# Kernel optimization log

Hardware: AMD Instinct MI355X
Metric: run time of the kernel (lower is better)

## Reference

```python
import jax, jax.numpy as jnp
import numpy as np

B, T, C, NH, HS, NL, VOCAB = 4, 1024, 768, 12, 64, 6, 128
PRIMES = [2, 3, 5, 7, 11, 13, 17, 19, 23, 29]
NEG_INF = jnp.finfo(jnp.float32).min


def _build_lut(t):
    # lut[n, i] = v_{p_i}(n), p-adic valuation of position n
    lut = np.zeros((t + 1, len(PRIMES)), np.float32)
    for pi, p in enumerate(PRIMES):
        nn = np.arange(t + 1, dtype=np.int64)
        nn[0] = 1  # v_p(0) treated as 0
        while (nn % p == 0).any():
            d = nn % p == 0
            lut[d, pi] += 1.0
            nn[d] //= p
    return lut


def _build_buffers(t):
    lut = _build_lut(t)
    vl = lut[1 : t + 1]  # positions 1..T, [T, 10]
    res = np.minimum(vl[:, None, :], vl[None, :, :]).sum(-1)  # [T, T]
    causal = np.tril(np.ones((t, t), dtype=bool))
    allowed = ((res > 0) | np.eye(t, dtype=bool)) & causal
    rbias = (np.log1p(res) * allowed).astype(np.float32)
    return vl.astype(np.float32), rbias, allowed


def setup_inputs() -> dict:
    key = jax.random.key(0)
    ks = jax.random.split(key, 16)
    s = 0.02
    vl, rbias, allowed = _build_buffers(T)
    return {
        "idx": jax.random.randint(ks[0], (B, T), 0, VOCAB, dtype=jnp.int32),
        "tok_emb": jax.random.normal(ks[1], (VOCAB, C)) * s,
        "pe_w": jax.random.normal(ks[2], (10, C)) * s,
        "pe_b": jnp.zeros((C,)),
        "vlut": jnp.asarray(vl),
        "rbias": jnp.asarray(rbias),
        "allowed": jnp.asarray(allowed),
        "ln1_g": jnp.ones((NL, C)),
        "ln1_b": jnp.zeros((NL, C)),
        "qw": jax.random.normal(ks[3], (NL, NH, C, HS)) * s,
        "kw": jax.random.normal(ks[4], (NL, NH, C, HS)) * s,
        "vw": jax.random.normal(ks[5], (NL, NH, C, HS)) * s,
        "proj_w": jax.random.normal(ks[6], (NL, C, C)) * s,
        "proj_b": jnp.zeros((NL, C)),
        "ln2_g": jnp.ones((NL, C)),
        "ln2_b": jnp.zeros((NL, C)),
        "ff1_w": jax.random.normal(ks[7], (NL, C, 4 * C)) * s,
        "ff1_b": jnp.zeros((NL, 4 * C)),
        "ff2_w": jax.random.normal(ks[8], (NL, 4 * C, C)) * s,
        "ff2_b": jnp.zeros((NL, C)),
        "lnf_g": jnp.ones((C,)),
        "lnf_b": jnp.zeros((C,)),
        "head_w": jax.random.normal(ks[9], (C, VOCAB)) * s,
        "head_b": jnp.zeros((VOCAB,)),
    }


def _ln(x, g, b, eps=1e-5):
    m = x.mean(-1, keepdims=True)
    v = ((x - m) ** 2).mean(-1, keepdims=True)
    return (x - m) * jax.lax.rsqrt(v + eps) * g + b


def reference(idx, tok_emb, pe_w, pe_b, vlut, rbias, allowed,
              ln1_g, ln1_b, qw, kw, vw, proj_w, proj_b,
              ln2_g, ln2_b, ff1_w, ff1_b, ff2_w, ff2_b,
              lnf_g, lnf_b, head_w, head_b):
    # token embedding + spectral positional encoding
    x = tok_emb[idx] + (vlut @ pe_w + pe_b)  # [B, T, C]
    scale = C ** (-0.5)  # NOTE: source scales by full embed dim, not head_size
    for l in range(NL):
        h = _ln(x, ln1_g[l], ln1_b[l])
        q = jnp.einsum("btc,hcd->bhtd", h, qw[l])
        k = jnp.einsum("btc,hcd->bhtd", h, kw[l])
        v = jnp.einsum("btc,hcd->bhtd", h, vw[l])
        w = jnp.einsum("bhtd,bhsd->bhts", q, k) * scale + rbias  # [B,H,T,T]
        w = jnp.where(allowed, w, NEG_INF)
        a = jax.nn.softmax(w, axis=-1)
        o = jnp.einsum("bhts,bhsd->bhtd", a, v)
        o = o.transpose(0, 2, 1, 3).reshape(x.shape[0], x.shape[1], C)
        x = x + o @ proj_w[l] + proj_b[l]
        h2 = _ln(x, ln2_g[l], ln2_b[l])
        x = x + jax.nn.gelu(h2 @ ff1_w[l] + ff1_b[l], approximate=False) @ ff2_w[l] + ff2_b[l]
    return _ln(x, lnf_g, lnf_b) @ head_w + head_b  # [B, T, VOCAB]
```

## Files before the change

### kernel.cpp

```cpp
#include <hip/hip_runtime.h>
#include <hip/hip_bf16.h>
#include <math.h>


#define Bz 4
#define Tz 1024
#define Cz 768
#define NHz 12
#define HSz 64
#define NLz 6
#define VOCABz 128
#define NTOK (Bz * Tz)

typedef __hip_bfloat16 bf16;
typedef __attribute__((ext_vector_type(8))) __bf16 bf16x8;
typedef __attribute__((ext_vector_type(4))) float f32x4;

#define MFMA16(a, b, c) __builtin_amdgcn_mfma_f32_16x16x32_bf16(a, b, c, 0, 0, 0)

__device__ __forceinline__ float bf2f(bf16 x) { return __bfloat162float(x); }
__device__ __forceinline__ bf16 f2bf(float x) { return __float2bfloat16(x); }
__device__ __forceinline__ float ldx(const void* p, size_t i, int f) {
  return f ? bf2f(((const bf16*)p)[i]) : ((const float*)p)[i];
}
__device__ __forceinline__ void async16(const bf16* g, bf16* l) {
  __builtin_amdgcn_global_load_lds(
      (const __attribute__((address_space(1))) unsigned int*)g,
      (__attribute__((address_space(3))) unsigned int*)l, 16, 0, 0);
}

__global__ void detect_kernel(const void* g1, int* flag) {
  if (threadIdx.x == 0) {
    const unsigned short* p = (const unsigned short*)g1;
    int cnt = 0;
    for (int i = 0; i < 64; i++) cnt += (p[i] == 0x3F80u) ? 1 : 0;
    *flag = (cnt >= 60) ? 1 : 0;
  }
}

__global__ __launch_bounds__(256) void convert_kernel(
    const void* __restrict__ src, bf16* __restrict__ dst, int n,
    const int* __restrict__ flagp) {
  int f = *flagp;
  int i = blockIdx.x * 256 + threadIdx.x;
  if (i >= n) return;
  dst[i] = f ? ((const bf16*)src)[i] : f2bf(((const float*)src)[i]);
}

__global__ __launch_bounds__(256) void transpose_tiled(
    const void* __restrict__ src, bf16* __restrict__ dst, int R, int C,
    size_t s_mat, size_t d_base, size_t d_l, size_t d_h, int hmod,
    const int* __restrict__ flagp) {
  __shared__ bf16 t[64][65];
  int f = *flagp;
  int c0 = blockIdx.x * 64, r0 = blockIdx.y * 64;
  int z = blockIdx.z;
  size_t so = (size_t)z * s_mat;
  size_t dofs = d_base + (size_t)(z / hmod) * d_l + (size_t)(z % hmod) * d_h;
  int tr = threadIdx.x >> 2;
  int tc = (threadIdx.x & 3) * 16;
  size_t sbase = so + (size_t)(r0 + tr) * C + c0 + tc;
#pragma unroll
  for (int u = 0; u < 16; u++) t[tr][tc + u] = f2bf(ldx(src, sbase + u, f));
  __syncthreads();
  int wc = threadIdx.x >> 2;
  int wr = (threadIdx.x & 3) * 16;
  bf16* dp = dst + dofs + (size_t)(c0 + wc) * R + r0 + wr;
#pragma unroll
  for (int u = 0; u < 16; u++) dp[u] = t[wr + u][wc];
}

__global__ __launch_bounds__(256) void embed_kernel(
    const int* __restrict__ idx, const bf16* __restrict__ tok_emb,
    const bf16* __restrict__ pe_w, const bf16* __restrict__ pe_b,
    const bf16* __restrict__ vlut, float* __restrict__ x_res) {
  int row = blockIdx.x;
  int t = row % Tz;
  int tok = idx[row];
  float vl[10];
#pragma unroll
  for (int p = 0; p < 10; p++) vl[p] = bf2f(vlut[t * 10 + p]);
  for (int c = threadIdx.x; c < Cz; c += 256) {
    float acc = bf2f(tok_emb[(size_t)tok * Cz + c]) + bf2f(pe_b[c]);
#pragma unroll
    for (int p = 0; p < 10; p++) acc += vl[p] * bf2f(pe_w[p * Cz + c]);
    x_res[(size_t)row * Cz + c] = acc;
  }
}

__global__ __launch_bounds__(256) void ln_kernel(
    const float* __restrict__ x, const bf16* __restrict__ g,
    const bf16* __restrict__ b, bf16* __restrict__ out) {
  __shared__ float r1[4], r2[4];
  int row = blockIdx.x, tid = threadIdx.x;
  const float* xr = x + (size_t)row * Cz;
  float v0 = xr[tid], v1 = xr[tid + 256], v2 = xr[tid + 512];
  float s1 = v0 + v1 + v2, s2 = v0 * v0 + v1 * v1 + v2 * v2;
#pragma unroll
  for (int off = 32; off > 0; off >>= 1) {
    s1 += __shfl_down(s1, off);
    s2 += __shfl_down(s2, off);
  }
  int lane = tid & 63, wid = tid >> 6;
  if (lane == 0) { r1[wid] = s1; r2[wid] = s2; }
  __syncthreads();
  s1 = r1[0] + r1[1] + r1[2] + r1[3];
  s2 = r2[0] + r2[1] + r2[2] + r2[3];
  float m = s1 * (1.0f / Cz);
  float var = s2 * (1.0f / Cz) - m * m;
  float inv = rsqrtf(var + 1e-5f);
  bf16* orow = out + (size_t)row * Cz;
  orow[tid] = f2bf((v0 - m) * inv * bf2f(g[tid]) + bf2f(b[tid]));
  orow[tid + 256] = f2bf((v1 - m) * inv * bf2f(g[tid + 256]) + bf2f(b[tid + 256]));
  orow[tid + 512] = f2bf((v2 - m) * inv * bf2f(g[tid + 512]) + bf2f(b[tid + 512]));
}

__global__ __launch_bounds__(256) void gemm_mfma(
    const bf16* __restrict__ A, const bf16* __restrict__ Wt,
    const bf16* __restrict__ bias, float* __restrict__ resid,
    void* __restrict__ out, int M, int N, int K, int mode,
    const int* __restrict__ flagp) {
  __shared__ bf16 lds[2][2][4096];
  int tid = threadIdx.x;
  int lane = tid & 63, w = tid >> 6;
  int wm = (w >> 1) * 64, wn = (w & 1) * 64;
  int q = lane >> 4, ln = lane & 15;
  int m0 = blockIdx.y * 128, n0 = blockIdx.x * 128;

  const bf16* gA[2];
  const bf16* gB[2];
#pragma unroll
  for (int p = 0; p < 2; p++) {
    int o = w * 2048 + p * 1024 + lane * 16;
    int rp = o >> 7, pp = (o >> 4) & 7;
    int pl = pp ^ (rp & 7);
    int row = rp * 2 + (pl >> 2);
    int cb = pl & 3;
    gA[p] = A + (size_t)(m0 + row) * K + cb * 8;
    gB[p] = Wt + (size_t)(n0 + row) * K + cb * 8;
  }
  int ppf = (((ln & 1) << 2) | q) ^ (ln >> 1);
  int aoff = wm * 32 + (ln >> 1) * 64 + ppf * 8;
  int boff = wn * 32 + (ln >> 1) * 64 + ppf * 8;

  f32x4 acc[4][4] = {};
#pragma unroll
  for (int p = 0; p < 2; p++) {
    async16(gA[p], &lds[0][0][w * 1024 + p * 512]);
    async16(gB[p], &lds[0][1][w * 1024 + p * 512]);
  }
  int cur = 0;
  for (int k0 = 0; k0 < K; k0 += 32) {
    __syncthreads();
    if (k0 + 32 < K) {
      int nxt = cur ^ 1;
#pragma unroll
      for (int p = 0; p < 2; p++) {
        async16(gA[p] + k0 + 32, &lds[nxt][0][w * 1024 + p * 512]);
        async16(gB[p] + k0 + 32, &lds[nxt][1][w * 1024 + p * 512]);
      }
    }
    bf16x8 af[4], bfr[4];
#pragma unroll
    for (int i = 0; i < 4; i++)
      af[i] = *(const bf16x8*)&lds[cur][0][aoff + i * 512];
#pragma unroll
    for (int j = 0; j < 4; j++)
      bfr[j] = *(const bf16x8*)&lds[cur][1][boff + j * 512];
#pragma unroll
    for (int i = 0; i < 4; i++)
#pragma unroll
      for (int j = 0; j < 4; j++)
        acc[i][j] = MFMA16(af[i], bfr[j], acc[i][j]);
    cur ^= 1;
  }
  int f = *flagp;
  float bj[4];
#pragma unroll
  for (int j = 0; j < 4; j++)
    bj[j] = bias ? bf2f(bias[n0 + wn + j * 16 + ln]) : 0.0f;
#pragma unroll
  for (int i = 0; i < 4; i++) {
#pragma unroll
    for (int j = 0; j < 4; j++) {
      int col = n0 + wn + j * 16 + ln;
#pragma unroll
      for (int r = 0; r < 4; r++) {
        int row = m0 + wm + i * 16 + q * 4 + r;
        float v = acc[i][j][r] + bj[j];
        size_t oi = (size_t)row * N + col;
        if (mode == 0) {
          ((bf16*)out)[oi] = f2bf(v);
        } else if (mode == 1) {
          ((bf16*)out)[oi] = f2bf(v * 0.5f * (1.0f + erff(v * 0.70710678118f)));
        } else if (mode == 2) {
          resid[oi] += v;
        } else {
          if (f) ((bf16*)out)[oi] = f2bf(v);
          else ((float*)out)[oi] = v;
        }
      }
    }
  }
}

#define ATS 72
__global__ __launch_bounds__(256) void transpose_v(
    const bf16* __restrict__ qkv, bf16* __restrict__ Vt) {
  __shared__ bf16 tile[64][ATS];
  int tid = threadIdx.x;
  int s0 = blockIdx.x * 64, bh = blockIdx.y;
  int b = bh / NHz, h = bh % NHz;
  int row = tid >> 2, c0 = (tid & 3) * 16;
  const bf16* src = qkv + ((size_t)(b * Tz + s0 + row)) * (3 * Cz) + 2 * Cz + h * HSz + c0;
  *(uint4*)&tile[row][c0] = *(const uint4*)src;
  *(uint4*)&tile[row][c0 + 8] = *(const uint4*)(src + 8);
  __syncthreads();
  int d = tid >> 2, sc0 = (tid & 3) * 16;
  unsigned int u[8];
#pragma unroll
  for (int m = 0; m < 8; m++) {
    unsigned int lo = *(const unsigned short*)&tile[sc0 + 2 * m][d];
    unsigned int hi = *(const unsigned short*)&tile[sc0 + 2 * m + 1][d];
    u[m] = lo | (hi << 16);
  }
  bf16* dst = Vt + ((size_t)bh * HSz + d) * Tz + s0 + sc0;
  ((uint4*)dst)[0] = make_uint4(u[0], u[1], u[2], u[3]);
  ((uint4*)dst)[1] = make_uint4(u[4], u[5], u[6], u[7]);
}

__global__ __launch_bounds__(256) void attn_flash(
    const bf16* __restrict__ qkv, const bf16* __restrict__ Vt,
    const bf16* __restrict__ rbias, bf16* __restrict__ attn_out) {
  __shared__ bf16 Qs[64][ATS];
  __shared__ bf16 Ks[64][ATS];
  __shared__ bf16 Vs[64][ATS];
  __shared__ bf16 Ps[4][16][ATS];
  int tid = threadIdx.x;
  int lane = tid & 63, w = tid >> 6;
  int q = lane >> 4, ln = lane & 15;
  int t0 = blockIdx.x * 64, bh = blockIdx.y;
  int b = bh / NHz, h = bh % NHz;
  const float scale = 0.03608439182435161f;
  int srow = tid >> 2, sc = (tid & 3) * 16;
  {
    const bf16* src = qkv + ((size_t)(b * Tz + t0 + srow)) * (3 * Cz) + h * HSz + sc;
    *(uint4*)&Qs[srow][sc] = *(const uint4*)src;
    *(uint4*)&Qs[srow][sc + 8] = *(const uint4*)(src + 8);
  }
  float mrow[4], lrow[4];
  f32x4 Oacc[4] = {};
#pragma unroll
  for (int r = 0; r < 4; r++) { mrow[r] = -3.0e38f; lrow[r] = 0.0f; }
  int t_base = t0 + w * 16 + q * 4;

  for (int s0 = 0; s0 <= t0 + 63; s0 += 64) {
    __syncthreads();
    {
      const bf16* ksrc = qkv + ((size_t)(b * Tz + s0 + srow)) * (3 * Cz) + Cz + h * HSz + sc;
      *(uint4*)&Ks[srow][sc] = *(const uint4*)ksrc;
      *(uint4*)&Ks[srow][sc + 8] = *(const uint4*)(ksrc + 8);
      const bf16* vsrc = Vt + ((size_t)bh * HSz + srow) * Tz + s0 + sc;
      *(uint4*)&Vs[srow][sc] = *(const uint4*)vsrc;
      *(uint4*)&Vs[srow][sc + 8] = *(const uint4*)(vsrc + 8);
    }
    __syncthreads();
    f32x4 sacc[4] = {};
#pragma unroll
    for (int ks = 0; ks < 64; ks += 32) {
      bf16x8 aq = *(const bf16x8*)&Qs[w * 16 + ln][ks + q * 8];
#pragma unroll
      for (int j = 0; j < 4; j++) {
        bf16x8 bk = *(const bf16x8*)&Ks[j * 16 + ln][ks + q * 8];
        sacc[j] = MFMA16(aq, bk, sacc[j]);
      }
    }
    float sval[4][4];
#pragma unroll
    for (int j = 0; j < 4; j++) {
      int s_col = s0 + j * 16 + ln;
#pragma unroll
      for (int r = 0; r < 4; r++) {
        int t_row = t_base + r;
        float rb = bf2f(rbias[(size_t)t_row * Tz + s_col]);
        float v = sacc[j][r] * scale + rb;
        bool ok = (s_col <= t_row) && ((rb > 0.0f) || (s_col == t_row));
        sval[j][r] = ok ? v : -3.0e38f;
      }
    }
    float rmax[4];
#pragma unroll
    for (int r = 0; r < 4; r++)
      rmax[r] = fmaxf(fmaxf(sval[0][r], sval[1][r]), fmaxf(sval[2][r], sval[3][r]));
#pragma unroll
    for (int msk = 8; msk >= 1; msk >>= 1)
#pragma unroll
      for (int r = 0; r < 4; r++)
        rmax[r] = fmaxf(rmax[r], __shfl_xor(rmax[r], msk));
    float nm[4], nme[4], alpha[4];
#pragma unroll
    for (int r = 0; r < 4; r++) {
      nm[r] = fmaxf(mrow[r], rmax[r]);
      nme[r] = (nm[r] < -1.0e37f) ? 0.0f : nm[r];
      alpha[r] = (mrow[r] < -1.0e37f) ? 0.0f : __expf(mrow[r] - nm[r]);
      mrow[r] = nm[r];
    }
    float pf[4][4];
    float psum[4] = {0.f, 0.f, 0.f, 0.f};
#pragma unroll
    for (int j = 0; j < 4; j++)
#pragma unroll
      for (int r = 0; r < 4; r++) {
        float p = __expf(sval[j][r] - nme[r]);
        pf[j][r] = p;
        psum[r] += p;
      }
#pragma unroll
    for (int msk = 8; msk >= 1; msk >>= 1)
#pragma unroll
      for (int r = 0; r < 4; r++) psum[r] += __shfl_xor(psum[r], msk);
#pragma unroll
    for (int r = 0; r < 4; r++) lrow[r] = alpha[r] * lrow[r] + psum[r];
#pragma unroll
    for (int jd = 0; jd < 4; jd++)
#pragma unroll
      for (int r = 0; r < 4; r++) Oacc[jd][r] *= alpha[r];
#pragma unroll
    for (int j = 0; j < 4; j++)
#pragma unroll
      for (int r = 0; r < 4; r++)
        Ps[w][q * 4 + r][j * 16 + ln] = f2bf(pf[j][r]);
#pragma unroll
    for (int ks = 0; ks < 64; ks += 32) {
      bf16x8 pa = *(const bf16x8*)&Ps[w][ln][ks + q * 8];
#pragma unroll
      for (int jd = 0; jd < 4; jd++) {
        bf16x8 vb = *(const bf16x8*)&Vs[jd * 16 + ln][ks + q * 8];
        Oacc[jd] = MFMA16(pa, vb, Oacc[jd]);
      }
    }
  }
#pragma unroll
  for (int r = 0; r < 4; r++) {
    float inv = 1.0f / lrow[r];
    int t_row = t_base + r;
#pragma unroll
    for (int jd = 0; jd < 4; jd++) {
      attn_out[(size_t)(b * Tz + t_row) * Cz + h * HSz + jd * 16 + ln] =
          f2bf(Oacc[jd][r] * inv);
    }
  }
}

extern "C" void kernel_launch(void* const* d_in, const int* in_sizes, int n_in,
                              void* d_out, int out_size, void* d_ws, size_t ws_size,
                              hipStream_t stream) {
  const int* idx = (const int*)d_in[0];
  int p0 = 7;
  if (n_in == 23) p0 = 6;
  else if (in_sizes[6] != Tz * Tz) p0 = 6;

  const void* r_tok_emb = d_in[1];
  const void* r_pe_w = d_in[2];
  const void* r_pe_b = d_in[3];
  const void* r_vlut = d_in[4];
  const void* r_rbias = d_in[5];
  const void* r_ln1_g = d_in[p0 + 0];
  const void* r_ln1_b = d_in[p0 + 1];
  const void* r_qw = d_in[p0 + 2];
  const void* r_kw = d_in[p0 + 3];
  const void* r_vw = d_in[p0 + 4];
  const void* r_proj_w = d_in[p0 + 5];
  const void* r_proj_b = d_in[p0 + 6];
  const void* r_ln2_g = d_in[p0 + 7];
  const void* r_ln2_b = d_in[p0 + 8];
  const void* r_ff1_w = d_in[p0 + 9];
  const void* r_ff1_b = d_in[p0 + 10];
  const void* r_ff2_w = d_in[p0 + 11];
  const void* r_ff2_b = d_in[p0 + 12];
  const void* r_lnf_g = d_in[p0 + 13];
  const void* r_lnf_b = d_in[p0 + 14];
  const void* r_head_w = d_in[p0 + 15];
  const void* r_head_b = d_in[p0 + 16];

  char* wsp = (char*)d_ws;
  auto alloc = [&](size_t bytes) {
    char* p = wsp;
    wsp += (bytes + 255) & ~(size_t)255;
    return (void*)p;
  };
  int* flag = (int*)alloc(256);
  float* x_res = (float*)alloc((size_t)NTOK * Cz * 4);
  bf16* h = (bf16*)alloc((size_t)NTOK * Cz * 2);
  bf16* qkv = (bf16*)alloc((size_t)NTOK * 3 * Cz * 2);
  bf16* attn = (bf16*)alloc((size_t)NTOK * Cz * 2);
  bf16* ffm = (bf16*)alloc((size_t)NTOK * 4 * Cz * 2);
  bf16* Vt = (bf16*)alloc((size_t)Bz * NHz * HSz * Tz * 2);
  bf16* wqkv_t = (bf16*)alloc((size_t)NLz * 3 * Cz * Cz * 2);
  bf16* proj_t = (bf16*)alloc((size_t)NLz * Cz * Cz * 2);
  bf16* ff1_t = (bf16*)alloc((size_t)NLz * 4 * Cz * Cz * 2);
  bf16* ff2_t = (bf16*)alloc((size_t)NLz * 4 * Cz * Cz * 2);
  bf16* head_t = (bf16*)alloc((size_t)VOCABz * Cz * 2);
  bf16* tok_emb = (bf16*)alloc((size_t)VOCABz * Cz * 2);
  bf16* pe_w = (bf16*)alloc(10 * Cz * 2);
  bf16* pe_b = (bf16*)alloc(Cz * 2);
  bf16* vlut = (bf16*)alloc(Tz * 10 * 2);
  bf16* rbias = (bf16*)alloc((size_t)Tz * Tz * 2);
  bf16* ln1_g = (bf16*)alloc(NLz * Cz * 2);
  bf16* ln1_b = (bf16*)alloc(NLz * Cz * 2);
  bf16* proj_b = (bf16*)alloc(NLz * Cz * 2);
  bf16* ln2_g = (bf16*)alloc(NLz * Cz * 2);
  bf16* ln2_b = (bf16*)alloc(NLz * Cz * 2);
  bf16* ff1_b = (bf16*)alloc(NLz * 4 * Cz * 2);
  bf16* ff2_b = (bf16*)alloc(NLz * Cz * 2);
  bf16* lnf_g = (bf16*)alloc(Cz * 2);
  bf16* lnf_b = (bf16*)alloc(Cz * 2);
  bf16* head_b = (bf16*)alloc(VOCABz * 2);

  detect_kernel<<<1, 64, 0, stream>>>(r_ln1_g, flag);

#define CONV(src, dst, n) \
  convert_kernel<<<((n) + 255) / 256, 256, 0, stream>>>(src, dst, n, flag)
  CONV(r_tok_emb, tok_emb, VOCABz * Cz);
  CONV(r_pe_w, pe_w, 10 * Cz);
  CONV(r_pe_b, pe_b, Cz);
  CONV(r_vlut, vlut, Tz * 10);
  CONV(r_rbias, rbias, Tz * Tz);
  CONV(r_ln1_g, ln1_g, NLz * Cz);
  CONV(r_ln1_b, ln1_b, NLz * Cz);
  CONV(r_proj_b, proj_b, NLz * Cz);
  CONV(r_ln2_g, ln2_g, NLz * Cz);
  CONV(r_ln2_b, ln2_b, NLz * Cz);
  CONV(r_ff1_b, ff1_b, NLz * 4 * Cz);
  CONV(r_ff2_b, ff2_b, NLz * Cz);
  CONV(r_lnf_g, lnf_g, Cz);
  CONV(r_lnf_b, lnf_b, Cz);
  CONV(r_head_b, head_b, VOCABz);
#undef CONV

  for (int g = 0; g < 3; g++) {
    const void* src = (g == 0) ? r_qw : (g == 1) ? r_kw : r_vw;
    transpose_tiled<<<dim3(1, Cz / 64, NLz * NHz), 256, 0, stream>>>(
        src, wqkv_t, Cz, HSz, (size_t)Cz * HSz,
        (size_t)g * Cz * Cz, (size_t)3 * Cz * Cz, (size_t)HSz * Cz, NHz, flag);
  }
  transpose_tiled<<<dim3(Cz / 64, Cz / 64, NLz), 256, 0, stream>>>(
      r_proj_w, proj_t, Cz, Cz, (size_t)Cz * Cz, 0, (size_t)Cz * Cz, 0, 1, flag);
  transpose_tiled<<<dim3(4 * Cz / 64, Cz / 64, NLz), 256, 0, stream>>>(
      r_ff1_w, ff1_t, Cz, 4 * Cz, (size_t)4 * Cz * Cz, 0, (size_t)4 * Cz * Cz, 0, 1, flag);
  transpose_tiled<<<dim3(Cz / 64, 4 * Cz / 64, NLz), 256, 0, stream>>>(
      r_ff2_w, ff2_t, 4 * Cz, Cz, (size_t)4 * Cz * Cz, 0, (size_t)4 * Cz * Cz, 0, 1, flag);
  transpose_tiled<<<dim3(VOCABz / 64, Cz / 64, 1), 256, 0, stream>>>(
      r_head_w, head_t, Cz, VOCABz, 0, 0, 0, 0, 1, flag);

  embed_kernel<<<NTOK, 256, 0, stream>>>(idx, tok_emb, pe_w, pe_b, vlut, x_res);

  for (int l = 0; l < NLz; l++) {
    ln_kernel<<<NTOK, 256, 0, stream>>>(x_res, ln1_g + l * Cz, ln1_b + l * Cz, h);
    gemm_mfma<<<dim3(3 * Cz / 128, NTOK / 128), 256, 0, stream>>>(
        h, wqkv_t + (size_t)l * 3 * Cz * Cz, nullptr, nullptr, qkv,
        NTOK, 3 * Cz, Cz, 0, flag);
    transpose_v<<<dim3(Tz / 64, Bz * NHz), 256, 0, stream>>>(qkv, Vt);
    attn_flash<<<dim3(Tz / 64, Bz * NHz), 256, 0, stream>>>(qkv, Vt, rbias, attn);
    gemm_mfma<<<dim3(Cz / 128, NTOK / 128), 256, 0, stream>>>(
        attn, proj_t + (size_t)l * Cz * Cz, proj_b + l * Cz, x_res, nullptr,
        NTOK, Cz, Cz, 2, flag);
    ln_kernel<<<NTOK, 256, 0, stream>>>(x_res, ln2_g + l * Cz, ln2_b + l * Cz, h);
    gemm_mfma<<<dim3(4 * Cz / 128, NTOK / 128), 256, 0, stream>>>(
        h, ff1_t + (size_t)l * 4 * Cz * Cz, ff1_b + (size_t)l * 4 * Cz, nullptr,
        ffm, NTOK, 4 * Cz, Cz, 1, flag);
    gemm_mfma<<<dim3(Cz / 128, NTOK / 128), 256, 0, stream>>>(
        ffm, ff2_t + (size_t)l * 4 * Cz * Cz, ff2_b + l * Cz, x_res, nullptr,
        NTOK, Cz, 4 * Cz, 2, flag);
  }
  ln_kernel<<<NTOK, 256, 0, stream>>>(x_res, lnf_g, lnf_b, h);
  gemm_mfma<<<dim3(VOCABz / 128, NTOK / 128), 256, 0, stream>>>(
      h, head_t, head_b, nullptr, d_out, NTOK, VOCABz, Cz, 3, flag);
}
```

Baseline: 1.875 ms.

## Template GEMM M-tile, enlarge attention query tile, batch conversion launches

The GEMM kernel is templated on its M tile, and the N=768 GEMMs (proj, ff2, head) now use 64-row tiles so more blocks are launched. Flash attention now handles 128 query rows per block, two 16-row groups per warp, which reuses each K/V tile across twice as many queries. Blocks are issued heaviest-first so the long causal tiles start early. The fifteen separate conversion kernels are merged into one grid-stride launch to cut launch overhead. Costs are more registers per attention thread and half as many attention blocks, which may lower occupancy.

```diff
diff --git a/kernel.cpp b/kernel.cpp
--- a/kernel.cpp
+++ b/kernel.cpp
@@ -38,13 +38,23 @@
   }
 }
 
-__global__ __launch_bounds__(256) void convert_kernel(
-    const void* __restrict__ src, bf16* __restrict__ dst, int n,
-    const int* __restrict__ flagp) {
+#define NCONV 15
+struct CPack {
+  const void* s[NCONV];
+  bf16* d[NCONV];
+  int n[NCONV];
+};
+__global__ __launch_bounds__(256) void convert_all(CPack p, const int* __restrict__ flagp) {
   int f = *flagp;
-  int i = blockIdx.x * 256 + threadIdx.x;
-  if (i >= n) return;
-  dst[i] = f ? ((const bf16*)src)[i] : f2bf(((const float*)src)[i]);
+  int stride = gridDim.x * 256;
+#pragma unroll 1
+  for (int t = 0; t < NCONV; t++) {
+    int n = p.n[t];
+    const void* src = p.s[t];
+    bf16* dst = p.d[t];
+    for (int i = blockIdx.x * 256 + threadIdx.x; i < n; i += stride)
+      dst[i] = f ? ((const bf16*)src)[i] : f2bf(((const float*)src)[i]);
+  }
 }
 
 __global__ __launch_bounds__(256) void transpose_tiled(
@@ -115,20 +125,33 @@
   orow[tid + 512] = f2bf((v2 - m) * inv * bf2f(g[tid + 512]) + bf2f(b[tid + 512]));
 }
 
+template <int MT>
 __global__ __launch_bounds__(256) void gemm_mfma(
     const bf16* __restrict__ A, const bf16* __restrict__ Wt,
     const bf16* __restrict__ bias, float* __restrict__ resid,
     void* __restrict__ out, int M, int N, int K, int mode,
     const int* __restrict__ flagp) {
-  __shared__ bf16 lds[2][2][4096];
+  constexpr int TM = MT * 32;
+  constexpr int API = MT / 2;
+  __shared__ bf16 ldsA[2][TM * 32];
+  __shared__ bf16 ldsB[2][4096];
   int tid = threadIdx.x;
   int lane = tid & 63, w = tid >> 6;
-  int wm = (w >> 1) * 64, wn = (w & 1) * 64;
+  int wm = (w >> 1) * (MT * 16), wn = (w & 1) * 64;
   int q = lane >> 4, ln = lane & 15;
-  int m0 = blockIdx.y * 128, n0 = blockIdx.x * 128;
-
-  const bf16* gA[2];
+  int m0 = blockIdx.y * TM, n0 = blockIdx.x * 128;
+
+  const bf16* gA[API];
   const bf16* gB[2];
+#pragma unroll
+  for (int p = 0; p < API; p++) {
+    int o = w * (API * 1024) + p * 1024 + lane * 16;
+    int rp = o >> 7, pp = (o >> 4) & 7;
+    int pl = pp ^ (rp & 7);
+    int row = rp * 2 + (pl >> 2);
+    int cb = pl & 3;
+    gA[p] = A + (size_t)(m0 + row) * K + cb * 8;
+  }
 #pragma unroll
   for (int p = 0; p < 2; p++) {
     int o = w * 2048 + p * 1024 + lane * 16;
@@ -136,39 +159,40 @@
     int pl = pp ^ (rp & 7);
     int row = rp * 2 + (pl >> 2);
     int cb = pl & 3;
-    gA[p] = A + (size_t)(m0 + row) * K + cb * 8;
     gB[p] = Wt + (size_t)(n0 + row) * K + cb * 8;
   }
   int ppf = (((ln & 1) << 2) | q) ^ (ln >> 1);
   int aoff = wm * 32 + (ln >> 1) * 64 + ppf * 8;
   int boff = wn * 32 + (ln >> 1) * 64 + ppf * 8;
 
-  f32x4 acc[4][4] = {};
-#pragma unroll
-  for (int p = 0; p < 2; p++) {
-    async16(gA[p], &lds[0][0][w * 1024 + p * 512]);
-    async16(gB[p], &lds[0][1][w * 1024 + p * 512]);
-  }
+  f32x4 acc[MT][4] = {};
+#pragma unroll
+  for (int p = 0; p < API; p++)
+    async16(gA[p], &ldsA[0][w * (API * 512) + p * 512]);
+#pragma unroll
+  for (int p = 0; p < 2; p++)
+    async16(gB[p], &ldsB[0][w * 1024 + p * 512]);
   int cur = 0;
   for (int k0 = 0; k0 < K; k0 += 32) {
     __syncthreads();
     if (k0 + 32 < K) {
       int nxt = cur ^ 1;
 #pragma unroll
-      for (int p = 0; p < 2; p++) {
-        async16(gA[p] + k0 + 32, &lds[nxt][0][w * 1024 + p * 512]);
-        async16(gB[p] + k0 + 32, &lds[nxt][1][w * 1024 + p * 512]);
-      }
-    }
-    bf16x8 af[4], bfr[4];
-#pragma unroll
-    for (int i = 0; i < 4; i++)
-      af[i] = *(const bf16x8*)&lds[cur][0][aoff + i * 512];
+      for (int p = 0; p < API; p++)
+        async16(gA[p] + k0 + 32, &ldsA[nxt][w * (API * 512) + p * 512]);
+#pragma unroll
+      for (int p = 0; p < 2; p++)
+        async16(gB[p] + k0 + 32, &ldsB[nxt][w * 1024 + p * 512]);
+    }
+    bf16x8 af[MT], bfr[4];
+#pragma unroll
+    for (int i = 0; i < MT; i++)
+      af[i] = *(const bf16x8*)&ldsA[cur][aoff + i * 512];
 #pragma unroll
     for (int j = 0; j < 4; j++)
-      bfr[j] = *(const bf16x8*)&lds[cur][1][boff + j * 512];
-#pragma unroll
-    for (int i = 0; i < 4; i++)
+      bfr[j] = *(const bf16x8*)&ldsB[cur][boff + j * 512];
+#pragma unroll
+    for (int i = 0; i < MT; i++)
 #pragma unroll
       for (int j = 0; j < 4; j++)
         acc[i][j] = MFMA16(af[i], bfr[j], acc[i][j]);
@@ -180,7 +204,7 @@
   for (int j = 0; j < 4; j++)
     bj[j] = bias ? bf2f(bias[n0 + wn + j * 16 + ln]) : 0.0f;
 #pragma unroll
-  for (int i = 0; i < 4; i++) {
+  for (int i = 0; i < MT; i++) {
 #pragma unroll
     for (int j = 0; j < 4; j++) {
       int col = n0 + wn + j * 16 + ln;
@@ -232,29 +256,35 @@
 __global__ __launch_bounds__(256) void attn_flash(
     const bf16* __restrict__ qkv, const bf16* __restrict__ Vt,
     const bf16* __restrict__ rbias, bf16* __restrict__ attn_out) {
-  __shared__ bf16 Qs[64][ATS];
+  __shared__ bf16 Qs[128][ATS];
   __shared__ bf16 Ks[64][ATS];
   __shared__ bf16 Vs[64][ATS];
-  __shared__ bf16 Ps[4][16][ATS];
+  __shared__ bf16 Ps[4][32][ATS];
   int tid = threadIdx.x;
   int lane = tid & 63, w = tid >> 6;
   int q = lane >> 4, ln = lane & 15;
-  int t0 = blockIdx.x * 64, bh = blockIdx.y;
+  int qt = 7 - blockIdx.x;
+  int t0 = qt * 128, bh = blockIdx.y;
   int b = bh / NHz, h = bh % NHz;
   const float scale = 0.03608439182435161f;
   int srow = tid >> 2, sc = (tid & 3) * 16;
-  {
-    const bf16* src = qkv + ((size_t)(b * Tz + t0 + srow)) * (3 * Cz) + h * HSz + sc;
-    *(uint4*)&Qs[srow][sc] = *(const uint4*)src;
-    *(uint4*)&Qs[srow][sc + 8] = *(const uint4*)(src + 8);
-  }
-  float mrow[4], lrow[4];
-  f32x4 Oacc[4] = {};
-#pragma unroll
-  for (int r = 0; r < 4; r++) { mrow[r] = -3.0e38f; lrow[r] = 0.0f; }
-  int t_base = t0 + w * 16 + q * 4;
-
-  for (int s0 = 0; s0 <= t0 + 63; s0 += 64) {
+#pragma unroll
+  for (int pass = 0; pass < 2; pass++) {
+    int r = srow + pass * 64;
+    const bf16* src = qkv + ((size_t)(b * Tz + t0 + r)) * (3 * Cz) + h * HSz + sc;
+    *(uint4*)&Qs[r][sc] = *(const uint4*)src;
+    *(uint4*)&Qs[r][sc + 8] = *(const uint4*)(src + 8);
+  }
+  float mrow[2][4], lrow[2][4];
+  f32x4 Oacc[2][4] = {};
+#pragma unroll
+  for (int i = 0; i < 2; i++)
+#pragma unroll
+    for (int r = 0; r < 4; r++) { mrow[i][r] = -3.0e38f; lrow[i][r] = 0.0f; }
+  int nk = 2 * qt + 2;
+
+  for (int kt = 0; kt < nk; kt++) {
+    int s0 = kt * 64;
     __syncthreads();
     {
       const bf16* ksrc = qkv + ((size_t)(b * Tz + s0 + srow)) * (3 * Cz) + Cz + h * HSz + sc;
@@ -265,91 +295,108 @@
       *(uint4*)&Vs[srow][sc + 8] = *(const uint4*)(vsrc + 8);
     }
     __syncthreads();
-    f32x4 sacc[4] = {};
+    f32x4 sacc[2][4] = {};
 #pragma unroll
     for (int ks = 0; ks < 64; ks += 32) {
-      bf16x8 aq = *(const bf16x8*)&Qs[w * 16 + ln][ks + q * 8];
+      bf16x8 aq[2];
+#pragma unroll
+      for (int i = 0; i < 2; i++)
+        aq[i] = *(const bf16x8*)&Qs[w * 32 + i * 16 + ln][ks + q * 8];
 #pragma unroll
       for (int j = 0; j < 4; j++) {
         bf16x8 bk = *(const bf16x8*)&Ks[j * 16 + ln][ks + q * 8];
-        sacc[j] = MFMA16(aq, bk, sacc[j]);
+#pragma unroll
+        for (int i = 0; i < 2; i++) sacc[i][j] = MFMA16(aq[i], bk, sacc[i][j]);
       }
     }
-    float sval[4][4];
-#pragma unroll
-    for (int j = 0; j < 4; j++) {
-      int s_col = s0 + j * 16 + ln;
+    float sval[2][4][4];
+#pragma unroll
+    for (int i = 0; i < 2; i++) {
+#pragma unroll
+      for (int j = 0; j < 4; j++) {
+        int s_col = s0 + j * 16 + ln;
+#pragma unroll
+        for (int r = 0; r < 4; r++) {
+          int t_row = t0 + w * 32 + i * 16 + q * 4 + r;
+          float rb = bf2f(rbias[(size_t)t_row * Tz + s_col]);
+          float v = sacc[i][j][r] * scale + rb;
+          bool ok = (s_col <= t_row) && ((rb > 0.0f) || (s_col == t_row));
+          sval[i][j][r] = ok ? v : -3.0e38f;
+        }
+      }
+    }
+    float pf[2][4][4];
+#pragma unroll
+    for (int i = 0; i < 2; i++) {
+      float rmax[4], psum[4];
+#pragma unroll
+      for (int r = 0; r < 4; r++)
+        rmax[r] = fmaxf(fmaxf(sval[i][0][r], sval[i][1][r]),
+                        fmaxf(sval[i][2][r], sval[i][3][r]));
+#pragma unroll
+      for (int msk = 8; msk >= 1; msk >>= 1)
+#pragma unroll
+        for (int r = 0; r < 4; r++)
+          rmax[r] = fmaxf(rmax[r], __shfl_xor(rmax[r], msk));
+      float nme[4], alpha[4];
 #pragma unroll
       for (int r = 0; r < 4; r++) {
-        int t_row = t_base + r;
-        float rb = bf2f(rbias[(size_t)t_row * Tz + s_col]);
-        float v = sacc[j][r] * scale + rb;
-        bool ok = (s_col <= t_row) && ((rb > 0.0f) || (s_col == t_row));
-        sval[j][r] = ok ? v : -3.0e38f;
+        float nm = fmaxf(mrow[i][r], rmax[r]);
+        nme[r] = (nm < -1.0e37f) ? 0.0f : nm;
+        alpha[r] = (mrow[i][r] < -1.0e37f) ? 0.0f : __expf(mrow[i][r] - nm);
+        mrow[i][r] = nm;
+        psum[r] = 0.0f;
       }
-    }
-    float rmax[4];
-#pragma unroll
-    for (int r = 0; r < 4; r++)
-      rmax[r] = fmaxf(fmaxf(sval[0][r], sval[1][r]), fmaxf(sval[2][r], sval[3][r]));
-#pragma unroll
-    for (int msk = 8; msk >= 1; msk >>= 1)
-#pragma unroll
-      for (int r = 0; r < 4; r++)
-        rmax[r] = fmaxf(rmax[r], __shfl_xor(rmax[r], msk));
-    float nm[4], nme[4], alpha[4];
-#pragma unroll
-    for (int r = 0; r < 4; r++) {
-      nm[r] = fmaxf(mrow[r], rmax[r]);
-      nme[r] = (nm[r] < -1.0e37f) ? 0.0f : nm[r];
-      alpha[r] = (mrow[r] < -1.0e37f) ? 0.0f : __expf(mrow[r] - nm[r]);
-      mrow[r] = nm[r];
-    }
-    float pf[4][4];
-    float psum[4] = {0.f, 0.f, 0.f, 0.f};
-#pragma unroll
-    for (int j = 0; j < 4; j++)
-#pragma unroll
-      for (int r = 0; r < 4; r++) {
-        float p = __expf(sval[j][r] - nme[r]);
-        pf[j][r] = p;
-        psum[r] += p;
-      }
-#pragma unroll
-    for (int msk = 8; msk >= 1; msk >>= 1)
-#pragma unroll
-      for (int r = 0; r < 4; r++) psum[r] += __shfl_xor(psum[r], msk);
-#pragma unroll
-    for (int r = 0; r < 4; r++) lrow[r] = alpha[r] * lrow[r] + psum[r];
-#pragma unroll
-    for (int jd = 0; jd < 4; jd++)
-#pragma unroll
-      for (int r = 0; r < 4; r++) Oacc[jd][r] *= alpha[r];
-#pragma unroll
-    for (int j = 0; j < 4; j++)
-#pragma unroll
-      for (int r = 0; r < 4; r++)
-        Ps[w][q * 4 + r][j * 16 + ln] = f2bf(pf[j][r]);
+#pragma unroll
+      for (int j = 0; j < 4; j++)
+#pragma unroll
+        for (int r = 0; r < 4; r++) {
+          float p = __expf(sval[i][j][r] - nme[r]);
+          pf[i][j][r] = p;
+          psum[r] += p;
+        }
+#pragma unroll
+      for (int msk = 8; msk >= 1; msk >>= 1)
+#pragma unroll
+        for (int r = 0; r < 4; r++) psum[r] += __shfl_xor(psum[r], msk);
+#pragma unroll
+      for (int r = 0; r < 4; r++) lrow[i][r] = alpha[r] * lrow[i][r] + psum[r];
+#pragma unroll
+      for (int jd = 0; jd < 4; jd++)
+#pragma unroll
+        for (int r = 0; r < 4; r++) Oacc[i][jd][r] *= alpha[r];
+#pragma unroll
+      for (int j = 0; j < 4; j++)
+#pragma unroll
+        for (int r = 0; r < 4; r++)
+          Ps[w][i * 16 + q * 4 + r][j * 16 + ln] = f2bf(pf[i][j][r]);
+    }
 #pragma unroll
     for (int ks = 0; ks < 64; ks += 32) {
-      bf16x8 pa = *(const bf16x8*)&Ps[w][ln][ks + q * 8];
+      bf16x8 pa[2];
+#pragma unroll
+      for (int i = 0; i < 2; i++)
+        pa[i] = *(const bf16x8*)&Ps[w][i * 16 + ln][ks + q * 8];
 #pragma unroll
       for (int jd = 0; jd < 4; jd++) {
         bf16x8 vb = *(const bf16x8*)&Vs[jd * 16 + ln][ks + q * 8];
-        Oacc[jd] = MFMA16(pa, vb, Oacc[jd]);
+#pragma unroll
+        for (int i = 0; i < 2; i++) Oacc[i][jd] = MFMA16(pa[i], vb, Oacc[i][jd]);
       }
     }
   }
 #pragma unroll
-  for (int r = 0; r < 4; r++) {
-    float inv = 1.0f / lrow[r];
-    int t_row = t_base + r;
-#pragma unroll
-    for (int jd = 0; jd < 4; jd++) {
-      attn_out[(size_t)(b * Tz + t_row) * Cz + h * HSz + jd * 16 + ln] =
-          f2bf(Oacc[jd][r] * inv);
-    }
-  }
+  for (int i = 0; i < 2; i++)
+#pragma unroll
+    for (int r = 0; r < 4; r++) {
+      float inv = 1.0f / lrow[i][r];
+      int t_row = t0 + w * 32 + i * 16 + q * 4 + r;
+#pragma unroll
+      for (int jd = 0; jd < 4; jd++) {
+        attn_out[(size_t)(b * Tz + t_row) * Cz + h * HSz + jd * 16 + ln] =
+            f2bf(Oacc[i][jd][r] * inv);
+      }
+    }
 }
 
 extern "C" void kernel_launch(void* const* d_in, const int* in_sizes, int n_in,
@@ -419,24 +466,18 @@
 
   detect_kernel<<<1, 64, 0, stream>>>(r_ln1_g, flag);
 
-#define CONV(src, dst, n) \
-  convert_kernel<<<((n) + 255) / 256, 256, 0, stream>>>(src, dst, n, flag)
-  CONV(r_tok_emb, tok_emb, VOCABz * Cz);
-  CONV(r_pe_w, pe_w, 10 * Cz);
-  CONV(r_pe_b, pe_b, Cz);
-  CONV(r_vlut, vlut, Tz * 10);
-  CONV(r_rbias, rbias, Tz * Tz);
-  CONV(r_ln1_g, ln1_g, NLz * Cz);
-  CONV(r_ln1_b, ln1_b, NLz * Cz);
-  CONV(r_proj_b, proj_b, NLz * Cz);
-  CONV(r_ln2_g, ln2_g, NLz * Cz);
-  CONV(r_ln2_b, ln2_b, NLz * Cz);
-  CONV(r_ff1_b, ff1_b, NLz * 4 * Cz);
-  CONV(r_ff2_b, ff2_b, NLz * Cz);
-  CONV(r_lnf_g, lnf_g, Cz);
-  CONV(r_lnf_b, lnf_b, Cz);
-  CONV(r_head_b, head_b, VOCABz);
-#undef CONV
+  CPack cp;
+  const void* csrc[NCONV] = {r_tok_emb, r_pe_w, r_pe_b, r_vlut, r_rbias,
+                             r_ln1_g, r_ln1_b, r_proj_b, r_ln2_g, r_ln2_b,
+                             r_ff1_b, r_ff2_b, r_lnf_g, r_lnf_b, r_head_b};
+  bf16* cdst[NCONV] = {tok_emb, pe_w, pe_b, vlut, rbias,
+                       ln1_g, ln1_b, proj_b, ln2_g, ln2_b,
+                       ff1_b, ff2_b, lnf_g, lnf_b, head_b};
+  int cn[NCONV] = {VOCABz * Cz, 10 * Cz, Cz, Tz * 10, Tz * Tz,
+                   NLz * Cz, NLz * Cz, NLz * Cz, NLz * Cz, NLz * Cz,
+                   NLz * 4 * Cz, NLz * Cz, Cz, Cz, VOCABz};
+  for (int i = 0; i < NCONV; i++) { cp.s[i] = csrc[i]; cp.d[i] = cdst[i]; cp.n[i] = cn[i]; }
+  convert_all<<<1024, 256, 0, stream>>>(cp, flag);
 
   for (int g = 0; g < 3; g++) {
     const void* src = (g == 0) ? r_qw : (g == 1) ? r_kw : r_vw;
@@ -457,23 +498,23 @@
 
   for (int l = 0; l < NLz; l++) {
     ln_kernel<<<NTOK, 256, 0, stream>>>(x_res, ln1_g + l * Cz, ln1_b + l * Cz, h);
-    gemm_mfma<<<dim3(3 * Cz / 128, NTOK / 128), 256, 0, stream>>>(
+    gemm_mfma<4><<<dim3(3 * Cz / 128, NTOK / 128), 256, 0, stream>>>(
         h, wqkv_t + (size_t)l * 3 * Cz * Cz, nullptr, nullptr, qkv,
         NTOK, 3 * Cz, Cz, 0, flag);
     transpose_v<<<dim3(Tz / 64, Bz * NHz), 256, 0, stream>>>(qkv, Vt);
-    attn_flash<<<dim3(Tz / 64, Bz * NHz), 256, 0, stream>>>(qkv, Vt, rbias, attn);
-    gemm_mfma<<<dim3(Cz / 128, NTOK / 128), 256, 0, stream>>>(
+    attn_flash<<<dim3(Tz / 128, Bz * NHz), 256, 0, stream>>>(qkv, Vt, rbias, attn);
+    gemm_mfma<2><<<dim3(Cz / 128, NTOK / 64), 256, 0, stream>>>(
         attn, proj_t + (size_t)l * Cz * Cz, proj_b + l * Cz, x_res, nullptr,
         NTOK, Cz, Cz, 2, flag);
     ln_kernel<<<NTOK, 256, 0, stream>>>(x_res, ln2_g + l * Cz, ln2_b + l * Cz, h);
-    gemm_mfma<<<dim3(4 * Cz / 128, NTOK / 128), 256, 0, stream>>>(
+    gemm_mfma<4><<<dim3(4 * Cz / 128, NTOK / 128), 256, 0, stream>>>(
         h, ff1_t + (size_t)l * 4 * Cz * Cz, ff1_b + (size_t)l * 4 * Cz, nullptr,
         ffm, NTOK, 4 * Cz, Cz, 1, flag);
-    gemm_mfma<<<dim3(Cz / 128, NTOK / 128), 256, 0, stream>>>(
+    gemm_mfma<2><<<dim3(Cz / 128, NTOK / 64), 256, 0, stream>>>(
         ffm, ff2_t + (size_t)l * 4 * Cz * Cz, ff2_b + l * Cz, x_res, nullptr,
         NTOK, Cz, 4 * Cz, 2, flag);
   }
   ln_kernel<<<NTOK, 256, 0, stream>>>(x_res, lnf_g, lnf_b, h);
-  gemm_mfma<<<dim3(VOCABz / 128, NTOK / 128), 256, 0, stream>>>(
+  gemm_mfma<2><<<dim3(VOCABz / 128, NTOK / 64), 256, 0, stream>>>(
       h, head_t, head_b, nullptr, d_out, NTOK, VOCABz, Cz, 3, flag);
 }
```

After: 2.116 ms. 12.9% more time.
